# Performance work log

Measured on AMD Instinct MI355X. Metric: run time of the kernel, lower is better.

## Reference

```python
import jax, jax.numpy as jnp
import numpy as np

NUM_HEADS = 8
MAXN = 1.0 - 1e-5        # ball projection radius for |k|=1
ATANH_CLIP = 1.0 - 1e-7  # artanh argument clamp (geoopt-style)
MIN_DEN = 1e-15

def _sqnorm(x):
    return jnp.sum(x * x, axis=-1, keepdims=True)

def _norm(x):
    return jnp.sqrt(jnp.clip(_sqnorm(x), MIN_DEN))

def artanh(x):
    return jnp.arctanh(jnp.clip(x, -ATANH_CLIP, ATANH_CLIP))

def project(x):
    n = _norm(x)
    return jnp.where(n > MAXN, x * (MAXN / n), x)

def mobius_add(x, y):
    # Mobius addition on Poincare ball, k=-1
    x2, y2 = _sqnorm(x), _sqnorm(y)
    xy = jnp.sum(x * y, axis=-1, keepdims=True)
    num = (1.0 + 2.0 * xy + y2) * x + (1.0 - x2) * y
    den = 1.0 + 2.0 * xy + x2 * y2
    return num / jnp.maximum(den, MIN_DEN)

def mobius_matvec(W, x):
    xn = jnp.clip(_norm(x), MIN_DEN)
    mx = x @ W.T
    mxn = jnp.clip(_norm(mx), MIN_DEN)
    res = jnp.tanh(mxn / xn * artanh(xn)) * (mx / mxn)
    zero = jnp.all(mx == 0, axis=-1, keepdims=True)
    return jnp.where(zero, jnp.zeros_like(res), res)

def mobius_linear(x, W, b):
    return project(mobius_add(mobius_matvec(W, x), b))

def logmap0(y):
    yn = jnp.clip(_norm(y), MIN_DEN)
    return artanh(yn) * y / yn

def expmap0(u):
    un = jnp.clip(_norm(u), MIN_DEN)
    return jnp.tanh(un) * u / un

def _fwd(query, key, value, Wq, bq, Wk, bk, Wv, bv, Wo, bo):
    B, S, D = query.shape
    dk = D // NUM_HEADS
    heads = lambda x: x.reshape(B, S, NUM_HEADS, dk).transpose(0, 2, 1, 3)
    Q = heads(mobius_linear(query, Wq, bq))  # (B,H,S,dk)
    K = heads(mobius_linear(key, Wk, bk))
    V = heads(mobius_linear(value, Wv, bv))
    # pairwise Poincare distance dist(q,k) = 2*artanh(||(-q) (+) k||),
    # expanded via dot products so we never build a (B,H,S,S,dk) tensor
    x2 = _sqnorm(Q)                          # (B,H,S,1)
    y2 = jnp.swapaxes(_sqnorm(K), -1, -2)    # (B,H,1,S)
    xy = jnp.einsum('bhid,bhjd->bhij', Q, K)
    A = 1.0 - 2.0 * xy + y2                  # coeff of (-q)
    Bc = 1.0 - x2                            # coeff of k
    num2 = A * A * x2 + Bc * Bc * y2 - 2.0 * A * Bc * xy
    den = jnp.maximum(1.0 - 2.0 * xy + x2 * y2, MIN_DEN)
    dist = 2.0 * artanh(jnp.sqrt(jnp.clip(num2, 0.0)) / den)
    scores = -dist / np.sqrt(dk).astype(np.float32)
    attn = jax.nn.softmax(scores, axis=-1)   # dropout skipped (eval/deterministic)
    # gyromidpoint weighted sum (vectorized form of the original python loops):
    # all softmax weights are > 0, so every j passes the >1e-10 branch
    w = attn / (jnp.sum(attn, axis=-1, keepdims=True) + 1e-10)
    mid = jnp.einsum('bhij,bhjd->bhid', w, logmap0(V))
    out = expmap0(mid)
    out = out.transpose(0, 2, 1, 3).reshape(B, S, D)
    return mobius_linear(out, Wo, bo), attn


def setup_inputs() -> dict:
    key = jax.random.key(0)
    ks = jax.random.split(key, 12)
    B, S, D = 2, 2048, 512
    pt = lambda k: project(0.05 * jax.random.normal(k, (B, S, D), dtype=jnp.float32))
    inp = {'query': pt(ks[0]), 'key': pt(ks[1]), 'value': pt(ks[2])}
    wscale = 1.0 / np.sqrt(D)
    for i, nm in enumerate(['q', 'k', 'v', 'o']):
        inp['W' + nm] = wscale * jax.random.normal(ks[3 + i], (D, D), dtype=jnp.float32)
        inp['b' + nm] = project(0.01 * jax.random.normal(ks[7 + i], (D,), dtype=jnp.float32))
    return inp


def reference(query, key, value, Wq, bq, Wk, bk, Wv, bv, Wo, bo):
    return _fwd(query, key, value, Wq, bq, Wk, bk, Wv, bv, Wo, bo)
```

## Files before the change

### kernel.cpp

```cpp
#include <hip/hip_runtime.h>
#include <math.h>

namespace {

constexpr int kB  = 2;
constexpr int kS  = 2048;
constexpr int kD  = 512;
constexpr int kH  = 8;
constexpr int kDK = 64;
constexpr int kM  = kB * kS;
constexpr int kBH = kB * kH;

typedef __attribute__((ext_vector_type(8))) short bf16x8;
typedef __attribute__((ext_vector_type(4))) float f32x4;

__device__ __forceinline__ float wave_sum64(float v) {
#pragma unroll
    for (int o = 32; o > 0; o >>= 1) v += __shfl_xor(v, o, 64);
    return v;
}

__device__ __forceinline__ unsigned short f2bf(float f) {
    unsigned u = __float_as_uint(f);
    unsigned r = (u + 0x7FFF + ((u >> 16) & 1)) >> 16;
    return (unsigned short)r;
}
__device__ __forceinline__ float bf2f(unsigned short h) {
    return __uint_as_float(((unsigned)h) << 16);
}

#define MAXN_F  ((float)(1.0 - 1e-5))
#define ACLIP_F ((float)(1.0 - 1e-7))

__global__ __launch_bounds__(256) void gemm_mfma(const float* __restrict__ X,
                                                 const float* __restrict__ W,
                                                 float* __restrict__ Y) {
    __shared__ unsigned short Ah[64 * 64], Al[64 * 64], Bh[64 * 64], Bl[64 * 64];
    const int m0 = blockIdx.x * 64;
    const int n0 = blockIdx.y * 64;
    const int tid = threadIdx.x;
    const int w = tid >> 6, l = tid & 63;
    const int lr = l & 15, lh = l >> 4;
    const int sr = tid >> 2;
    const int sk = (tid & 3) * 16;
    float4 xr[4], wr[4];
#pragma unroll
    for (int i = 0; i < 4; ++i) {
        xr[i] = *(const float4*)(X + (size_t)(m0 + sr) * 512 + sk + i * 4);
        wr[i] = *(const float4*)(W + (size_t)(n0 + sr) * 512 + sk + i * 4);
    }
    f32x4 acc[4];
#pragma unroll
    for (int j = 0; j < 4; ++j) acc[j] = (f32x4){0.f, 0.f, 0.f, 0.f};

    for (int c = 0; c < 8; ++c) {
        if (c) __syncthreads();
        {
            unsigned hx[8], lx[8], hw_[8], lw_[8];
#pragma unroll
            for (int t = 0; t < 8; ++t) {
                float e0 = ((const float*)&xr[t >> 1])[(t & 1) * 2 + 0];
                float e1 = ((const float*)&xr[t >> 1])[(t & 1) * 2 + 1];
                unsigned short h0 = f2bf(e0), h1 = f2bf(e1);
                hx[t] = (unsigned)h0 | ((unsigned)h1 << 16);
                lx[t] = (unsigned)f2bf(e0 - bf2f(h0)) | ((unsigned)f2bf(e1 - bf2f(h1)) << 16);
                float f0 = ((const float*)&wr[t >> 1])[(t & 1) * 2 + 0];
                float f1 = ((const float*)&wr[t >> 1])[(t & 1) * 2 + 1];
                unsigned short g0 = f2bf(f0), g1 = f2bf(f1);
                hw_[t] = (unsigned)g0 | ((unsigned)g1 << 16);
                lw_[t] = (unsigned)f2bf(f0 - bf2f(g0)) | ((unsigned)f2bf(f1 - bf2f(g1)) << 16);
            }
            const int ga = (sk >> 3) ^ (sr & 7);
            const int gb = ((sk >> 3) + 1) ^ (sr & 7);
            *(uint4*)&Ah[sr * 64 + ga * 8] = make_uint4(hx[0], hx[1], hx[2], hx[3]);
            *(uint4*)&Ah[sr * 64 + gb * 8] = make_uint4(hx[4], hx[5], hx[6], hx[7]);
            *(uint4*)&Al[sr * 64 + ga * 8] = make_uint4(lx[0], lx[1], lx[2], lx[3]);
            *(uint4*)&Al[sr * 64 + gb * 8] = make_uint4(lx[4], lx[5], lx[6], lx[7]);
            *(uint4*)&Bh[sr * 64 + ga * 8] = make_uint4(hw_[0], hw_[1], hw_[2], hw_[3]);
            *(uint4*)&Bh[sr * 64 + gb * 8] = make_uint4(hw_[4], hw_[5], hw_[6], hw_[7]);
            *(uint4*)&Bl[sr * 64 + ga * 8] = make_uint4(lw_[0], lw_[1], lw_[2], lw_[3]);
            *(uint4*)&Bl[sr * 64 + gb * 8] = make_uint4(lw_[4], lw_[5], lw_[6], lw_[7]);
        }
        if (c < 7) {
            const int k1 = (c + 1) * 64;
#pragma unroll
            for (int i = 0; i < 4; ++i) {
                xr[i] = *(const float4*)(X + (size_t)(m0 + sr) * 512 + k1 + sk + i * 4);
                wr[i] = *(const float4*)(W + (size_t)(n0 + sr) * 512 + k1 + sk + i * 4);
            }
        }
        __syncthreads();
#pragma unroll
        for (int ks = 0; ks < 2; ++ks) {
            const int kb = ks * 4 + lh;
            const int row = w * 16 + lr;
            const int aoff = row * 64 + ((kb ^ (row & 7)) << 3);
            bf16x8 ah = *(const bf16x8*)&Ah[aoff];
            bf16x8 al = *(const bf16x8*)&Al[aoff];
#pragma unroll
            for (int fn = 0; fn < 4; ++fn) {
                const int col = fn * 16 + lr;
                const int boff = col * 64 + ((kb ^ (col & 7)) << 3);
                bf16x8 bh8 = *(const bf16x8*)&Bh[boff];
                bf16x8 bl8 = *(const bf16x8*)&Bl[boff];
                acc[fn] = __builtin_amdgcn_mfma_f32_16x16x32_bf16(ah, bh8, acc[fn], 0, 0, 0);
                acc[fn] = __builtin_amdgcn_mfma_f32_16x16x32_bf16(al, bh8, acc[fn], 0, 0, 0);
                acc[fn] = __builtin_amdgcn_mfma_f32_16x16x32_bf16(ah, bl8, acc[fn], 0, 0, 0);
            }
        }
    }
#pragma unroll
    for (int fn = 0; fn < 4; ++fn)
#pragma unroll
        for (int r = 0; r < 4; ++r)
            Y[(size_t)(m0 + w * 16 + lh * 4 + r) * 512 + n0 + fn * 16 + lr] = acc[fn][r];
}

__global__ __launch_bounds__(256) void rowops(const float* __restrict__ X,
                                              const float* __restrict__ MX,
                                              const float* __restrict__ bvec,
                                              float* __restrict__ out) {
    __shared__ float4 red4[4];
    __shared__ float red1[4];
    const int row = blockIdx.x;
    const int tid = threadIdx.x;
    const float2 xv = ((const float2*)(X + (size_t)row * kD))[tid];
    const float2 mv = ((const float2*)(MX + (size_t)row * kD))[tid];
    const float2 bv = ((const float2*)bvec)[tid];
    float sx  = fmaf(xv.x, xv.x, xv.y * xv.y);
    float sm  = fmaf(mv.x, mv.x, mv.y * mv.y);
    float smb = fmaf(mv.x, bv.x, mv.y * bv.y);
    float sb  = fmaf(bv.x, bv.x, bv.y * bv.y);
#pragma unroll
    for (int o = 32; o > 0; o >>= 1) {
        sx  += __shfl_xor(sx, o, 64);
        sm  += __shfl_xor(sm, o, 64);
        smb += __shfl_xor(smb, o, 64);
        sb  += __shfl_xor(sb, o, 64);
    }
    if ((tid & 63) == 0) red4[tid >> 6] = make_float4(sx, sm, smb, sb);
    __syncthreads();
    {
        float4 r0 = red4[0], r1 = red4[1], r2 = red4[2], r3 = red4[3];
        sx  = r0.x + r1.x + r2.x + r3.x;
        sm  = r0.y + r1.y + r2.y + r3.y;
        smb = r0.z + r1.z + r2.z + r3.z;
        sb  = r0.w + r1.w + r2.w + r3.w;
    }
    float xn  = sqrtf(fmaxf(sx, 1e-15f));
    float mxn = sqrtf(fmaxf(sm, 1e-15f));
    float xc  = fminf(xn, ACLIP_F);
    float at  = 0.5f * logf((1.f + xc) / (1.f - xc));
    float sc  = tanhf(mxn / xn * at) / mxn;
    if (sm == 0.f) sc = 0.f;
    float x2 = sc * sc * sm;
    float xy = sc * smb;
    float y2 = sb;
    float c1 = 1.f + 2.f * xy + y2;
    float c2 = 1.f - x2;
    float den = fmaxf(1.f + 2.f * xy + x2 * y2, 1e-15f);
    float idn = 1.f / den;
    float ux = (c1 * sc * mv.x + c2 * bv.x) * idn;
    float uy = (c1 * sc * mv.y + c2 * bv.y) * idn;
    float su = wave_sum64(fmaf(ux, ux, uy * uy));
    if ((tid & 63) == 0) red1[tid >> 6] = su;
    __syncthreads();
    su = (red1[0] + red1[1]) + (red1[2] + red1[3]);
    float n = sqrtf(fmaxf(su, 1e-15f));
    float f = (n > MAXN_F) ? (MAXN_F / n) : 1.f;
    ((float2*)(out + (size_t)row * kD))[tid] = make_float2(ux * f, uy * f);
}

__global__ __launch_bounds__(256) void prep2(const float* __restrict__ Qp,
                                             const float* __restrict__ Kp,
                                             const float* __restrict__ Vp,
                                             float* __restrict__ qn2,
                                             float* __restrict__ kn2,
                                             unsigned short* __restrict__ LVbT) {
    __shared__ unsigned short T[64][66];
    const int bh = blockIdx.x >> 5;
    const int k0 = (blockIdx.x & 31) * 64;
    const int b = bh >> 3, h = bh & 7;
    const int w = threadIdx.x >> 6, l = threadIdx.x & 63;
#pragma unroll 4
    for (int i = 0; i < 16; ++i) {
        const int s = k0 + w * 16 + i;
        const size_t src = (size_t)(b * kS + s) * kD + h * kDK + l;
        float qv = Qp[src], kv = Kp[src], vv = Vp[src];
        float sq = wave_sum64(qv * qv);
        float sk = wave_sum64(kv * kv);
        float sv = wave_sum64(vv * vv);
        if (l == 0) { qn2[(bh << 11) + s] = sq; kn2[(bh << 11) + s] = sk; }
        float yn = sqrtf(fmaxf(sv, 1e-15f));
        float yc = fminf(yn, ACLIP_F);
        float coef = 0.5f * logf((1.f + yc) / (1.f - yc)) / yn;
        T[l][w * 16 + i] = f2bf(vv * coef);
    }
    __syncthreads();
    const int n = threadIdx.x >> 2, kk = (threadIdx.x & 3) * 16;
    const unsigned int* Tr = (const unsigned int*)&T[n][kk];
    unsigned int u0 = Tr[0], u1 = Tr[1], u2 = Tr[2], u3 = Tr[3];
    unsigned int u4 = Tr[4], u5 = Tr[5], u6 = Tr[6], u7 = Tr[7];
    unsigned short* dst = LVbT + (((size_t)(bh * 64 + n)) << 11) + k0 + kk;
    *(uint4*)dst = make_uint4(u0, u1, u2, u3);
    *(uint4*)(dst + 8) = make_uint4(u4, u5, u6, u7);
}

__global__ __launch_bounds__(256) void split_qk(const float* __restrict__ Qp,
                                                const float* __restrict__ Kp,
                                                unsigned short* __restrict__ Qhi,
                                                unsigned short* __restrict__ Qlo,
                                                unsigned short* __restrict__ Khi,
                                                unsigned short* __restrict__ Klo) {
    const int gid  = blockIdx.x * 4 + (threadIdx.x >> 6);
    const int lane = threadIdx.x & 63;
    const int bh = gid >> 11, s = gid & 2047;
    const int b = bh >> 3, h = bh & 7;
    const size_t src = (size_t)(b * kS + s) * kD + h * kDK + lane;
    const size_t dst = ((size_t)gid << 6) + lane;
    float qv = Qp[src];
    unsigned short qh = f2bf(qv);
    Qhi[dst] = qh;
    Qlo[dst] = f2bf(qv - bf2f(qh));
    float kv = Kp[src];
    unsigned short kh = f2bf(kv);
    Khi[dst] = kh;
    Klo[dst] = f2bf(kv - bf2f(kh));
}

__global__ __launch_bounds__(256) void fused_attn(const unsigned short* __restrict__ Qhi,
                                                  const unsigned short* __restrict__ Qlo,
                                                  const unsigned short* __restrict__ Khi,
                                                  const unsigned short* __restrict__ Klo,
                                                  const unsigned short* __restrict__ LVbT,
                                                  const float* __restrict__ qn2,
                                                  const float* __restrict__ kn2,
                                                  float* __restrict__ attn,
                                                  float* __restrict__ outcat) {
    __shared__ unsigned short KshH[64 * 64], KshL[64 * 64], LVsh[64 * 64], Psh[32 * 64];
    __shared__ float rsL[4][32], nsL[4][32];
    __shared__ float invSL[32], coefL[32];
    unsigned short* eattn = (unsigned short*)attn;

    const int wgid = blockIdx.x;
    const int x = wgid & 7, bq_ = wgid >> 3;
    const int bh = 2 * x + (bq_ >> 6);
    const int i0 = (bq_ & 63) * 32;
    const int b = bh >> 3, h = bh & 7;
    const int tid = threadIdx.x;
    const int w = tid >> 6, l = tid & 63;
    const int lr = l & 15, lh = l >> 4;
    const int srj = tid >> 2;
    const int skk = (tid & 3) * 16;
    const size_t kvbase = ((size_t)(bh << 11)) << 6;
    const size_t lvbase = ((size_t)bh) << 17;

    bf16x8 qah[2][2], qal[2][2];
#pragma unroll
    for (int fm = 0; fm < 2; ++fm)
#pragma unroll
        for (int ks = 0; ks < 2; ++ks) {
            const size_t a = ((size_t)(bh << 11) + i0 + fm * 16 + lr) * 64 + (ks * 4 + lh) * 8;
            qah[fm][ks] = *(const bf16x8*)&Qhi[a];
            qal[fm][ks] = *(const bf16x8*)&Qlo[a];
        }
    float4 x2q[2];
    x2q[0] = *(const float4*)(qn2 + (bh << 11) + i0 + 0 * 16 + lh * 4);
    x2q[1] = *(const float4*)(qn2 + (bh << 11) + i0 + 1 * 16 + lh * 4);

    const int ga = (((skk >> 3) ^ (srj & 7)) << 3);
    const int gb = ((((skk >> 3) + 1) ^ (srj & 7)) << 3);
    const int jc = w * 16 + lr;
    uint4 pA0, pA1, pB0, pB1, pC0, pC1;
    {
        const unsigned short* kh = Khi + kvbase + (size_t)srj * 64 + skk;
        const unsigned short* kl = Klo + kvbase + (size_t)srj * 64 + skk;
        const unsigned short* lv = LVbT + lvbase + (size_t)srj * 2048 + skk;
        pA0 = *(const uint4*)kh; pA1 = *(const uint4*)(kh + 8);
        pB0 = *(const uint4*)kl; pB1 = *(const uint4*)(kl + 8);
        pC0 = *(const uint4*)lv; pC1 = *(const uint4*)(lv + 8);
    }

    f32x4 pvacc[2];
    pvacc[0] = (f32x4){0.f, 0.f, 0.f, 0.f};
    pvacc[1] = (f32x4){0.f, 0.f, 0.f, 0.f};
    float rsp[2][4] = {};

    for (int t = 0; t < 32; ++t) {
        const int j0 = t * 64;
        const float y2 = kn2[(bh << 11) + j0 + jc];
        if (t) __syncthreads();
        *(uint4*)&KshH[srj * 64 + ga] = pA0; *(uint4*)&KshH[srj * 64 + gb] = pA1;
        *(uint4*)&KshL[srj * 64 + ga] = pB0; *(uint4*)&KshL[srj * 64 + gb] = pB1;
        *(uint4*)&LVsh[srj * 64 + ga] = pC0; *(uint4*)&LVsh[srj * 64 + gb] = pC1;
        if (t < 31) {
            const unsigned short* kh = Khi + kvbase + (size_t)(j0 + 64 + srj) * 64 + skk;
            const unsigned short* kl = Klo + kvbase + (size_t)(j0 + 64 + srj) * 64 + skk;
            const unsigned short* lv = LVbT + lvbase + (size_t)srj * 2048 + j0 + 64 + skk;
            pA0 = *(const uint4*)kh; pA1 = *(const uint4*)(kh + 8);
            pB0 = *(const uint4*)kl; pB1 = *(const uint4*)(kl + 8);
            pC0 = *(const uint4*)lv; pC1 = *(const uint4*)(lv + 8);
        }
        __syncthreads();
        f32x4 sacc[2];
        sacc[0] = (f32x4){0.f, 0.f, 0.f, 0.f};
        sacc[1] = (f32x4){0.f, 0.f, 0.f, 0.f};
#pragma unroll
        for (int ks = 0; ks < 2; ++ks) {
            const int kb = ks * 4 + lh;
            const int boff = jc * 64 + ((kb ^ (jc & 7)) << 3);
            bf16x8 bh8 = *(const bf16x8*)&KshH[boff];
            bf16x8 bl8 = *(const bf16x8*)&KshL[boff];
#pragma unroll
            for (int fm = 0; fm < 2; ++fm) {
                sacc[fm] = __builtin_amdgcn_mfma_f32_16x16x32_bf16(qah[fm][ks], bh8, sacc[fm], 0, 0, 0);
                sacc[fm] = __builtin_amdgcn_mfma_f32_16x16x32_bf16(qal[fm][ks], bh8, sacc[fm], 0, 0, 0);
                sacc[fm] = __builtin_amdgcn_mfma_f32_16x16x32_bf16(qah[fm][ks], bl8, sacc[fm], 0, 0, 0);
            }
        }
        const int pg = jc >> 3, pw = jc & 7;
#pragma unroll
        for (int fm = 0; fm < 2; ++fm)
#pragma unroll
            for (int r = 0; r < 4; ++r) {
                const int row = fm * 16 + lh * 4 + r;
                float xy = sacc[fm][r];
                float x2 = ((const float*)&x2q[fm])[r];
                float A_ = 1.f - 2.f * xy + y2;
                float Bc = 1.f - x2;
                float num2 = A_ * A_ * x2 + Bc * Bc * y2 - 2.f * A_ * Bc * xy;
                float den  = fmaxf(1.f - 2.f * xy + x2 * y2, 1e-15f);
                float sn   = __builtin_amdgcn_sqrtf(fmaxf(num2, 0.f));
                float dm   = den - sn;
                dm = fmaxf(dm, (den + sn) * 5e-8f);
                float rr = (den + sn) * __builtin_amdgcn_rcpf(dm);
                float e = __builtin_amdgcn_exp2f(-0.125f * __builtin_amdgcn_logf(rr));
                rsp[fm][r] += e;
                Psh[row * 64 + ((pg ^ (row & 7)) << 3) + pw] = f2bf(e);
            }
        __syncthreads();
#pragma unroll
        for (int ks = 0; ks < 2; ++ks) {
            const int kb = ks * 4 + lh;
            bf16x8 bv8 = *(const bf16x8*)&LVsh[jc * 64 + ((kb ^ (jc & 7)) << 3)];
#pragma unroll
            for (int fm = 0; fm < 2; ++fm) {
                const int prow = fm * 16 + lr;
                bf16x8 pa = *(const bf16x8*)&Psh[prow * 64 + ((kb ^ (prow & 7)) << 3)];
                pvacc[fm] = __builtin_amdgcn_mfma_f32_16x16x32_bf16(pa, bv8, pvacc[fm], 0, 0, 0);
            }
        }
        {
            const int prow = tid >> 3, g = tid & 7;
            uint4 ev = *(const uint4*)&Psh[prow * 64 + ((g ^ (prow & 7)) << 3)];
            *(uint4*)(eattn + ((size_t)(bh << 11) + i0 + prow) * 4096 + j0 + g * 8) = ev;
        }
    }
    __syncthreads();
#pragma unroll
    for (int fm = 0; fm < 2; ++fm)
#pragma unroll
        for (int r = 0; r < 4; ++r) {
            float v = rsp[fm][r];
            v += __shfl_xor(v, 1, 64); v += __shfl_xor(v, 2, 64);
            v += __shfl_xor(v, 4, 64); v += __shfl_xor(v, 8, 64);
            rsp[fm][r] = v;
        }
    if (lr == 0) {
#pragma unroll
        for (int fm = 0; fm < 2; ++fm)
#pragma unroll
            for (int r = 0; r < 4; ++r) rsL[w][fm * 16 + lh * 4 + r] = rsp[fm][r];
    }
    __syncthreads();
    if (tid < 32)
        invSL[tid] = 1.f / (rsL[0][tid] + rsL[1][tid] + rsL[2][tid] + rsL[3][tid]);
    __syncthreads();
    float mval[2][4];
#pragma unroll
    for (int fm = 0; fm < 2; ++fm)
#pragma unroll
        for (int r = 0; r < 4; ++r) {
            const int row = fm * 16 + lh * 4 + r;
            float m = pvacc[fm][r] * invSL[row];
            mval[fm][r] = m;
            float ns = m * m;
            ns += __shfl_xor(ns, 1, 64); ns += __shfl_xor(ns, 2, 64);
            ns += __shfl_xor(ns, 4, 64); ns += __shfl_xor(ns, 8, 64);
            if (lr == 0) nsL[w][row] = ns;
        }
    __syncthreads();
    if (tid < 32) {
        float ns = nsL[0][tid] + nsL[1][tid] + nsL[2][tid] + nsL[3][tid];
        float un = sqrtf(fmaxf(ns, 1e-15f));
        coefL[tid] = tanhf(un) / un;
    }
    __syncthreads();
#pragma unroll
    for (int fm = 0; fm < 2; ++fm)
#pragma unroll
        for (int r = 0; r < 4; ++r) {
            const int row = fm * 16 + lh * 4 + r;
            outcat[(size_t)(b * kS + i0 + row) * kD + h * kDK + jc] = mval[fm][r] * coefL[row];
        }

    for (int r = 0; r < 32; r += 2) {
        const size_t rb0 = (size_t)(bh << 11) + i0 + r;
        const size_t rb1 = rb0 + 1;
        uint4 ev0 = *(const uint4*)(eattn + rb0 * 4096 + tid * 8);
        uint4 ev1 = *(const uint4*)(eattn + rb1 * 4096 + tid * 8);
        const float is0 = invSL[r];
        const float is1 = invSL[r + 1];
        __syncthreads();
        float o[8];
        o[0] = __uint_as_float(ev0.x << 16) * is0;
        o[1] = __uint_as_float(ev0.x & 0xFFFF0000u) * is0;
        o[2] = __uint_as_float(ev0.y << 16) * is0;
        o[3] = __uint_as_float(ev0.y & 0xFFFF0000u) * is0;
        o[4] = __uint_as_float(ev0.z << 16) * is0;
        o[5] = __uint_as_float(ev0.z & 0xFFFF0000u) * is0;
        o[6] = __uint_as_float(ev0.w << 16) * is0;
        o[7] = __uint_as_float(ev0.w & 0xFFFF0000u) * is0;
        float* d0 = attn + rb0 * kS + tid * 8;
        *(float4*)d0       = make_float4(o[0], o[1], o[2], o[3]);
        *(float4*)(d0 + 4) = make_float4(o[4], o[5], o[6], o[7]);
        o[0] = __uint_as_float(ev1.x << 16) * is1;
        o[1] = __uint_as_float(ev1.x & 0xFFFF0000u) * is1;
        o[2] = __uint_as_float(ev1.y << 16) * is1;
        o[3] = __uint_as_float(ev1.y & 0xFFFF0000u) * is1;
        o[4] = __uint_as_float(ev1.z << 16) * is1;
        o[5] = __uint_as_float(ev1.z & 0xFFFF0000u) * is1;
        o[6] = __uint_as_float(ev1.w << 16) * is1;
        o[7] = __uint_as_float(ev1.w & 0xFFFF0000u) * is1;
        float* d1 = attn + rb1 * kS + tid * 8;
        *(float4*)d1       = make_float4(o[0], o[1], o[2], o[3]);
        *(float4*)(d1 + 4) = make_float4(o[4], o[5], o[6], o[7]);
    }
}

}

extern "C" void kernel_launch(void* const* d_in, const int* in_sizes, int n_in,
                              void* d_out, int out_size, void* d_ws, size_t ws_size,
                              hipStream_t stream) {
    const float* q  = (const float*)d_in[0];
    const float* k  = (const float*)d_in[1];
    const float* v  = (const float*)d_in[2];
    const float* Wq = (const float*)d_in[3];
    const float* bq = (const float*)d_in[4];
    const float* Wk = (const float*)d_in[5];
    const float* bk = (const float*)d_in[6];
    const float* Wv = (const float*)d_in[7];
    const float* bv = (const float*)d_in[8];
    const float* Wo = (const float*)d_in[9];
    const float* bo = (const float*)d_in[10];

    float* out  = (float*)d_out;
    float* attn = out + (size_t)kM * kD;

    constexpr size_t NBUF = (size_t)kM * kD;
    float* ws  = (float*)d_ws;
    float* A0  = ws;
    float* A1  = ws + NBUF;
    float* A2  = ws + 2 * NBUF;
    float* A3  = ws + 3 * NBUF;
    float* qn2 = ws + 4 * NBUF;
    float* kn2 = qn2 + (size_t)kBH * kS;

    constexpr size_t HP = (size_t)kBH * kS * kDK;
    unsigned short* Qhi = (unsigned short*)A2;
    unsigned short* Qlo = Qhi + HP;
    unsigned short* Khi = (unsigned short*)out;
    unsigned short* Klo = Khi + HP;
    unsigned short* LVbT = (unsigned short*)A3;

    dim3 gg(kM / 64, kD / 64);

    gemm_mfma<<<gg, 256, 0, stream>>>(q, Wq, A3);
    rowops<<<kM, 256, 0, stream>>>(q, A3, bq, A0);
    gemm_mfma<<<gg, 256, 0, stream>>>(k, Wk, A3);
    rowops<<<kM, 256, 0, stream>>>(k, A3, bk, A1);
    gemm_mfma<<<gg, 256, 0, stream>>>(v, Wv, A3);
    rowops<<<kM, 256, 0, stream>>>(v, A3, bv, A2);

    prep2<<<kBH * 32, 256, 0, stream>>>(A0, A1, A2, qn2, kn2, LVbT);

    split_qk<<<(kBH * kS) / 4, 256, 0, stream>>>(A0, A1, Qhi, Qlo, Khi, Klo);

    fused_attn<<<kBH * (kS / 32), 256, 0, stream>>>(Qhi, Qlo, Khi, Klo, LVbT,
                                                    qn2, kn2, attn, A1);

    gemm_mfma<<<gg, 256, 0, stream>>>(A1, Wo, A2);
    rowops<<<kM, 256, 0, stream>>>(A1, A2, bo, out);
}
```

Measured before the change: 290.1 us.

## Keep softmax probabilities in registers for PV MFMA, removing per-tile barrier

Swaps the MFMA operand order for QK^T so each lane holds scores for one query row across four keys. Those scores are packed straight into a zero-padded bf16 A fragment for the P·V MFMA, so the mid-tile barrier and LDS round trip of P are no longer needed. Each wave now accumulates partial P·V over its own 16 keys for all 64 output dims, and the four wave partials are reduced through shared memory at the end. The attention-row flush to global moves to the start of the next iteration. In exchange it runs twice as many PV MFMAs with half-empty K operands and uses more accumulator registers.

New measurement: 278.8 us. 3.9% less time.

```diff
diff --git a/kernel.cpp b/kernel.cpp
--- a/kernel.cpp
+++ b/kernel.cpp
@@ -27,6 +27,12 @@
 }
 __device__ __forceinline__ float bf2f(unsigned short h) {
     return __uint_as_float(((unsigned)h) << 16);
+}
+
+__device__ __forceinline__ bf16x8 mk_bf8(unsigned p0, unsigned p1) {
+    union { unsigned u[4]; bf16x8 v; } t;
+    t.u[0] = p0; t.u[1] = p1; t.u[2] = 0; t.u[3] = 0;
+    return t.v;
 }
 
 #define MAXN_F  ((float)(1.0 - 1e-5))
@@ -237,9 +243,14 @@
                                                   const float* __restrict__ kn2,
                                                   float* __restrict__ attn,
                                                   float* __restrict__ outcat) {
-    __shared__ unsigned short KshH[64 * 64], KshL[64 * 64], LVsh[64 * 64], Psh[32 * 64];
-    __shared__ float rsL[4][32], nsL[4][32];
-    __shared__ float invSL[32], coefL[32];
+    __shared__ unsigned long long smem_raw[4096];
+    unsigned short* KshH = (unsigned short*)smem_raw;
+    unsigned short* KshL = KshH + 4096;
+    unsigned short* LVsh = KshL + 4096;
+    unsigned short* Psh  = LVsh + 4096;
+    float* Pmid = (float*)smem_raw;
+    __shared__ float rsL[4][32];
+    __shared__ float invSL[32];
     unsigned short* eattn = (unsigned short*)attn;
 
     const int wgid = blockIdx.x;
@@ -264,13 +275,14 @@
             qah[fm][ks] = *(const bf16x8*)&Qhi[a];
             qal[fm][ks] = *(const bf16x8*)&Qlo[a];
         }
-    float4 x2q[2];
-    x2q[0] = *(const float4*)(qn2 + (bh << 11) + i0 + 0 * 16 + lh * 4);
-    x2q[1] = *(const float4*)(qn2 + (bh << 11) + i0 + 1 * 16 + lh * 4);
+    float x2s[2];
+    x2s[0] = qn2[(bh << 11) + i0 + 0 * 16 + lr];
+    x2s[1] = qn2[(bh << 11) + i0 + 1 * 16 + lr];
 
     const int ga = (((skk >> 3) ^ (srj & 7)) << 3);
     const int gb = ((((skk >> 3) + 1) ^ (srj & 7)) << 3);
-    const int jc = w * 16 + lr;
+    const int jrow = w * 16 + lr;
+    const int aoff0 = jrow * 64;
     uint4 pA0, pA1, pB0, pB1, pC0, pC1;
     {
         const unsigned short* kh = Khi + kvbase + (size_t)srj * 64 + skk;
@@ -281,15 +293,25 @@
         pC0 = *(const uint4*)lv; pC1 = *(const uint4*)(lv + 8);
     }
 
-    f32x4 pvacc[2];
-    pvacc[0] = (f32x4){0.f, 0.f, 0.f, 0.f};
-    pvacc[1] = (f32x4){0.f, 0.f, 0.f, 0.f};
-    float rsp[2][4] = {};
+    f32x4 pvacc[2][4];
+#pragma unroll
+    for (int fm = 0; fm < 2; ++fm)
+#pragma unroll
+        for (int g2 = 0; g2 < 4; ++g2) pvacc[fm][g2] = (f32x4){0.f, 0.f, 0.f, 0.f};
+    float rsp[2] = {0.f, 0.f};
+
+    const int fl_row = tid >> 3, fl_g = tid & 7;
+    const int pgj = w * 2 + (lh >> 1);
+    const int pjo = (lh & 1) * 4;
 
     for (int t = 0; t < 32; ++t) {
         const int j0 = t * 64;
-        const float y2 = kn2[(bh << 11) + j0 + jc];
-        if (t) __syncthreads();
+        __syncthreads();
+        if (t) {
+            uint4 ev = *(const uint4*)&Psh[fl_row * 64 + ((fl_g ^ (fl_row & 7)) << 3)];
+            *(uint4*)(eattn + ((size_t)(bh << 11) + i0 + fl_row) * 4096 +
+                      (j0 - 64) + fl_g * 8) = ev;
+        }
         *(uint4*)&KshH[srj * 64 + ga] = pA0; *(uint4*)&KshH[srj * 64 + gb] = pA1;
         *(uint4*)&KshL[srj * 64 + ga] = pB0; *(uint4*)&KshL[srj * 64 + gb] = pB1;
         *(uint4*)&LVsh[srj * 64 + ga] = pC0; *(uint4*)&LVsh[srj * 64 + gb] = pC1;
@@ -308,24 +330,26 @@
 #pragma unroll
         for (int ks = 0; ks < 2; ++ks) {
             const int kb = ks * 4 + lh;
-            const int boff = jc * 64 + ((kb ^ (jc & 7)) << 3);
-            bf16x8 bh8 = *(const bf16x8*)&KshH[boff];
-            bf16x8 bl8 = *(const bf16x8*)&KshL[boff];
+            const int aoff = aoff0 + ((kb ^ (jrow & 7)) << 3);
+            bf16x8 kh8 = *(const bf16x8*)&KshH[aoff];
+            bf16x8 kl8 = *(const bf16x8*)&KshL[aoff];
 #pragma unroll
             for (int fm = 0; fm < 2; ++fm) {
-                sacc[fm] = __builtin_amdgcn_mfma_f32_16x16x32_bf16(qah[fm][ks], bh8, sacc[fm], 0, 0, 0);
-                sacc[fm] = __builtin_amdgcn_mfma_f32_16x16x32_bf16(qal[fm][ks], bh8, sacc[fm], 0, 0, 0);
-                sacc[fm] = __builtin_amdgcn_mfma_f32_16x16x32_bf16(qah[fm][ks], bl8, sacc[fm], 0, 0, 0);
+                sacc[fm] = __builtin_amdgcn_mfma_f32_16x16x32_bf16(kh8, qah[fm][ks], sacc[fm], 0, 0, 0);
+                sacc[fm] = __builtin_amdgcn_mfma_f32_16x16x32_bf16(kh8, qal[fm][ks], sacc[fm], 0, 0, 0);
+                sacc[fm] = __builtin_amdgcn_mfma_f32_16x16x32_bf16(kl8, qah[fm][ks], sacc[fm], 0, 0, 0);
             }
         }
-        const int pg = jc >> 3, pw = jc & 7;
-#pragma unroll
-        for (int fm = 0; fm < 2; ++fm)
+        float4 y2v = *(const float4*)(kn2 + (bh << 11) + j0 + w * 16 + lh * 4);
+        bf16x8 ebf[2];
+#pragma unroll
+        for (int fm = 0; fm < 2; ++fm) {
+            const float x2 = x2s[fm];
+            float es[4];
 #pragma unroll
             for (int r = 0; r < 4; ++r) {
-                const int row = fm * 16 + lh * 4 + r;
                 float xy = sacc[fm][r];
-                float x2 = ((const float*)&x2q[fm])[r];
+                float y2 = ((const float*)&y2v)[r];
                 float A_ = 1.f - 2.f * xy + y2;
                 float Bc = 1.f - x2;
                 float num2 = A_ * A_ * x2 + Bc * Bc * y2 - 2.f * A_ * Bc * xy;
@@ -335,75 +359,75 @@
                 dm = fmaxf(dm, (den + sn) * 5e-8f);
                 float rr = (den + sn) * __builtin_amdgcn_rcpf(dm);
                 float e = __builtin_amdgcn_exp2f(-0.125f * __builtin_amdgcn_logf(rr));
-                rsp[fm][r] += e;
-                Psh[row * 64 + ((pg ^ (row & 7)) << 3) + pw] = f2bf(e);
+                es[r] = e;
+                rsp[fm] += e;
             }
-        __syncthreads();
-#pragma unroll
-        for (int ks = 0; ks < 2; ++ks) {
-            const int kb = ks * 4 + lh;
-            bf16x8 bv8 = *(const bf16x8*)&LVsh[jc * 64 + ((kb ^ (jc & 7)) << 3)];
-#pragma unroll
-            for (int fm = 0; fm < 2; ++fm) {
-                const int prow = fm * 16 + lr;
-                bf16x8 pa = *(const bf16x8*)&Psh[prow * 64 + ((kb ^ (prow & 7)) << 3)];
-                pvacc[fm] = __builtin_amdgcn_mfma_f32_16x16x32_bf16(pa, bv8, pvacc[fm], 0, 0, 0);
-            }
-        }
-        {
-            const int prow = tid >> 3, g = tid & 7;
-            uint4 ev = *(const uint4*)&Psh[prow * 64 + ((g ^ (prow & 7)) << 3)];
-            *(uint4*)(eattn + ((size_t)(bh << 11) + i0 + prow) * 4096 + j0 + g * 8) = ev;
-        }
-    }
-    __syncthreads();
+            unsigned p0 = (unsigned)f2bf(es[0]) | ((unsigned)f2bf(es[1]) << 16);
+            unsigned p1 = (unsigned)f2bf(es[2]) | ((unsigned)f2bf(es[3]) << 16);
+            ebf[fm] = mk_bf8(p0, p1);
+            const int prow = fm * 16 + lr;
+            *(uint2*)&Psh[prow * 64 + ((pgj ^ (prow & 7)) << 3) + pjo] = make_uint2(p0, p1);
+        }
+#pragma unroll
+        for (int g2 = 0; g2 < 4; ++g2) {
+            const int dk = g2 * 16 + lr;
+            uint2 lvp = *(const uint2*)&LVsh[dk * 64 + ((pgj ^ (dk & 7)) << 3) + pjo];
+            bf16x8 bfr = mk_bf8(lvp.x, lvp.y);
+            pvacc[0][g2] = __builtin_amdgcn_mfma_f32_16x16x32_bf16(ebf[0], bfr, pvacc[0][g2], 0, 0, 0);
+            pvacc[1][g2] = __builtin_amdgcn_mfma_f32_16x16x32_bf16(ebf[1], bfr, pvacc[1][g2], 0, 0, 0);
+        }
+    }
+    __syncthreads();
+    {
+        uint4 ev = *(const uint4*)&Psh[fl_row * 64 + ((fl_g ^ (fl_row & 7)) << 3)];
+        *(uint4*)(eattn + ((size_t)(bh << 11) + i0 + fl_row) * 4096 + 31 * 64 + fl_g * 8) = ev;
+    }
+#pragma unroll
+    for (int fm = 0; fm < 2; ++fm) {
+        rsp[fm] += __shfl_xor(rsp[fm], 16, 64);
+        rsp[fm] += __shfl_xor(rsp[fm], 32, 64);
+    }
+    __syncthreads();
+    if (l < 16) { rsL[w][l] = rsp[0]; rsL[w][16 + l] = rsp[1]; }
 #pragma unroll
     for (int fm = 0; fm < 2; ++fm)
 #pragma unroll
-        for (int r = 0; r < 4; ++r) {
-            float v = rsp[fm][r];
-            v += __shfl_xor(v, 1, 64); v += __shfl_xor(v, 2, 64);
-            v += __shfl_xor(v, 4, 64); v += __shfl_xor(v, 8, 64);
-            rsp[fm][r] = v;
-        }
-    if (lr == 0) {
-#pragma unroll
-        for (int fm = 0; fm < 2; ++fm)
-#pragma unroll
-            for (int r = 0; r < 4; ++r) rsL[w][fm * 16 + lh * 4 + r] = rsp[fm][r];
-    }
+        for (int g2 = 0; g2 < 4; ++g2)
+#pragma unroll
+            for (int r = 0; r < 4; ++r)
+                Pmid[w * 2048 + (fm * 16 + lh * 4 + r) * 64 + g2 * 16 + lr] = pvacc[fm][g2][r];
     __syncthreads();
     if (tid < 32)
         invSL[tid] = 1.f / (rsL[0][tid] + rsL[1][tid] + rsL[2][tid] + rsL[3][tid]);
     __syncthreads();
-    float mval[2][4];
-#pragma unroll
-    for (int fm = 0; fm < 2; ++fm)
-#pragma unroll
-        for (int r = 0; r < 4; ++r) {
-            const int row = fm * 16 + lh * 4 + r;
-            float m = pvacc[fm][r] * invSL[row];
-            mval[fm][r] = m;
-            float ns = m * m;
-            ns += __shfl_xor(ns, 1, 64); ns += __shfl_xor(ns, 2, 64);
-            ns += __shfl_xor(ns, 4, 64); ns += __shfl_xor(ns, 8, 64);
-            if (lr == 0) nsL[w][row] = ns;
-        }
-    __syncthreads();
-    if (tid < 32) {
-        float ns = nsL[0][tid] + nsL[1][tid] + nsL[2][tid] + nsL[3][tid];
+    {
+        const int q = tid >> 3;
+        const int c8 = (tid & 7) * 8;
+        float m[8];
+#pragma unroll
+        for (int i = 0; i < 8; i += 4) {
+            float4 a0 = *(const float4*)&Pmid[0 * 2048 + q * 64 + c8 + i];
+            float4 a1 = *(const float4*)&Pmid[1 * 2048 + q * 64 + c8 + i];
+            float4 a2 = *(const float4*)&Pmid[2 * 2048 + q * 64 + c8 + i];
+            float4 a3 = *(const float4*)&Pmid[3 * 2048 + q * 64 + c8 + i];
+            m[i + 0] = (a0.x + a1.x) + (a2.x + a3.x);
+            m[i + 1] = (a0.y + a1.y) + (a2.y + a3.y);
+            m[i + 2] = (a0.z + a1.z) + (a2.z + a3.z);
+            m[i + 3] = (a0.w + a1.w) + (a2.w + a3.w);
+        }
+        const float is = invSL[q];
+        float ns = 0.f;
+#pragma unroll
+        for (int i = 0; i < 8; ++i) { m[i] *= is; ns = fmaf(m[i], m[i], ns); }
+        ns += __shfl_xor(ns, 1, 64);
+        ns += __shfl_xor(ns, 2, 64);
+        ns += __shfl_xor(ns, 4, 64);
         float un = sqrtf(fmaxf(ns, 1e-15f));
-        coefL[tid] = tanhf(un) / un;
-    }
-    __syncthreads();
-#pragma unroll
-    for (int fm = 0; fm < 2; ++fm)
-#pragma unroll
-        for (int r = 0; r < 4; ++r) {
-            const int row = fm * 16 + lh * 4 + r;
-            outcat[(size_t)(b * kS + i0 + row) * kD + h * kDK + jc] = mval[fm][r] * coefL[row];
-        }
-
+        float coef = tanhf(un) / un;
+        float* dst = outcat + (size_t)(b * kS + i0 + q) * kD + h * kDK + c8;
+        *(float4*)dst       = make_float4(m[0] * coef, m[1] * coef, m[2] * coef, m[3] * coef);
+        *(float4*)(dst + 4) = make_float4(m[4] * coef, m[5] * coef, m[6] * coef, m[7] * coef);
+    }
     for (int r = 0; r < 32; r += 2) {
         const size_t rb0 = (size_t)(bh << 11) + i0 + r;
         const size_t rb1 = rb0 + 1;
```
